# Kernel optimization log

Hardware: AMD Instinct MI355X
Metric: run time of the kernel (lower is better)

The kernel has to match this reference:

```python
import jax, jax.numpy as jnp
import numpy as np

EMBED = 768
HEADS = 12
HEAD_DIM = EMBED // HEADS
HIDDEN = 4 * EMBED


def layer_norm(x, gamma, beta, eps=1e-5):
    mu = jnp.mean(x, axis=-1, keepdims=True)
    var = jnp.var(x, axis=-1, keepdims=True)
    return (x - mu) * jax.lax.rsqrt(var + eps) * gamma + beta


def setup_inputs() -> dict:
    key = jax.random.key(0)
    ks = jax.random.split(key, 10)
    B, N, C = 64, 577, EMBED
    s_in = 1.0 / np.sqrt(C)
    s_hid = 1.0 / np.sqrt(HIDDEN)
    return {
        "x": jax.random.normal(ks[0], (B, N, C), jnp.float32),
        "ln1_g": jnp.ones((C,), jnp.float32),
        "ln1_b": jnp.zeros((C,), jnp.float32),
        "w_qkv": jax.random.normal(ks[1], (C, 3 * C), jnp.float32) * s_in,  # no bias (qkv_bias=False)
        "w_proj": jax.random.normal(ks[2], (C, C), jnp.float32) * s_in,
        "b_proj": jnp.zeros((C,), jnp.float32),
        "ln2_g": jnp.ones((C,), jnp.float32),
        "ln2_b": jnp.zeros((C,), jnp.float32),
        "w_fc1": jax.random.normal(ks[3], (C, HIDDEN), jnp.float32) * s_in,
        "b_fc1": jnp.zeros((HIDDEN,), jnp.float32),
        "w_fc2": jax.random.normal(ks[4], (HIDDEN, C), jnp.float32) * s_hid,
        "b_fc2": jnp.zeros((C,), jnp.float32),
    }


def reference(x, ln1_g, ln1_b, w_qkv, w_proj, b_proj, ln2_g, ln2_b, w_fc1, b_fc1, w_fc2, b_fc2):
    B, N, C = x.shape
    # --- attention branch (pre-norm) ---
    h = layer_norm(x, ln1_g, ln1_b)
    qkv = (h @ w_qkv).reshape(B, N, 3, HEADS, HEAD_DIM)
    q = jnp.transpose(qkv[:, :, 0], (0, 2, 1, 3))  # [B,H,N,D]
    k = jnp.transpose(qkv[:, :, 1], (0, 2, 1, 3))
    v = jnp.transpose(qkv[:, :, 2], (0, 2, 1, 3))
    scale = HEAD_DIM ** -0.5
    att = jax.nn.softmax(jnp.einsum("bhnd,bhmd->bhnm", q, k) * scale, axis=-1)
    o = jnp.einsum("bhnm,bhmd->bhnd", att, v)
    o = jnp.transpose(o, (0, 2, 1, 3)).reshape(B, N, C)
    x = x + (o @ w_proj + b_proj)
    # --- MLP branch (pre-norm) ---
    h = layer_norm(x, ln2_g, ln2_b)
    h = jax.nn.gelu(h @ w_fc1 + b_fc1, approximate=False)
    x = x + (h @ w_fc2 + b_fc2)
    return x
```

## Files before the change

### kernel.cpp

```cpp
#include <hip/hip_runtime.h>
#include <hip/hip_bf16.h>
#include <math.h>

using bf16 = __hip_bfloat16;
typedef __attribute__((ext_vector_type(8))) short short8;
typedef __attribute__((ext_vector_type(4))) float f32x4;

#define NSEQ   577
#define NBATCH 64
#define NTOK   36928
#define MPAD   37120
#define NHEADS 12
#define HDIM   64
#define NP     640
#define CEMB   768
#define CHID   3072
#define NBH    (NBATCH*NHEADS)

__device__ __forceinline__ bf16 f2bf(float v){ return __float2bfloat16(v); }

__device__ __forceinline__ float gelu_f(float x) {
    float x3 = x * x * x;
    float y = 1.5957691216057308f * (x + 0.044715f * x3);
    float e = __expf(y);
    float t = 1.0f - 2.0f / (e + 1.0f);
    return 0.5f * x * (1.0f + t);
}

#define GLOAD_LDS16(gaddr, laddr) \
  __builtin_amdgcn_global_load_lds((__attribute__((address_space(1))) const void*)(gaddr), \
                                   (__attribute__((address_space(3))) void*)(laddr), 16, 0, 0)

__global__ __launch_bounds__(256) void transpose_w(const float* __restrict__ src,
                                                   bf16* __restrict__ dst, int R, int C) {
    long idx = (long)blockIdx.x * 256 + threadIdx.x;
    long total = (long)R * C;
    if (idx < total) {
        int r = (int)(idx / C);
        int c = (int)(idx - (long)r * C);
        dst[(long)c * R + r] = f2bf(src[idx]);
    }
}

__global__ __launch_bounds__(256) void ln_kernel(const float* __restrict__ x,
                                                 const float* __restrict__ gamma,
                                                 const float* __restrict__ beta,
                                                 bf16* __restrict__ out) {
    int row = blockIdx.x;
    const float* xr = x + (size_t)row * CEMB;
    int tid = threadIdx.x;
    float v0 = xr[tid], v1 = xr[tid + 256], v2 = xr[tid + 512];
    float s = v0 + v1 + v2;
    #pragma unroll
    for (int o = 32; o > 0; o >>= 1) s += __shfl_down(s, o);
    __shared__ float red[4];
    if ((tid & 63) == 0) red[tid >> 6] = s;
    __syncthreads();
    float mean = (red[0] + red[1] + red[2] + red[3]) * (1.0f / CEMB);
    float d0 = v0 - mean, d1 = v1 - mean, d2 = v2 - mean;
    float q = d0*d0 + d1*d1 + d2*d2;
    #pragma unroll
    for (int o = 32; o > 0; o >>= 1) q += __shfl_down(q, o);
    __shared__ float red2[4];
    if ((tid & 63) == 0) red2[tid >> 6] = q;
    __syncthreads();
    float var = (red2[0] + red2[1] + red2[2] + red2[3]) * (1.0f / CEMB);
    float rs = rsqrtf(var + 1e-5f);
    bf16* orow = out + (size_t)row * CEMB;
    orow[tid]       = f2bf(d0 * rs * gamma[tid]       + beta[tid]);
    orow[tid + 256] = f2bf(d1 * rs * gamma[tid + 256] + beta[tid + 256]);
    orow[tid + 512] = f2bf(d2 * rs * gamma[tid + 512] + beta[tid + 512]);
}

__global__ __launch_bounds__(256) void flash_attn(const bf16* __restrict__ qg,
                                                  const bf16* __restrict__ kg,
                                                  const bf16* __restrict__ vtg,
                                                  bf16* __restrict__ og) {
    const int tid = threadIdx.x, lane = tid & 63, w = tid >> 6;
    const int fr = lane & 15, fh = lane >> 4;
    const int bh = blockIdx.y;
    const int q0 = blockIdx.x * 128;
    const int wr = w * 32;

    __shared__ bf16 Ks[64 * 64];
    __shared__ bf16 Vs[64 * 64];
    __shared__ bf16 Ps[128 * 64];

    const bf16* qb = qg  + (size_t)bh * NP * HDIM;
    const bf16* kb = kg  + (size_t)bh * NP * HDIM;
    const bf16* vb = vtg + (size_t)bh * HDIM * NP;

    short8 qa[2][2];
    #pragma unroll
    for (int mi = 0; mi < 2; mi++)
        #pragma unroll
        for (int ks = 0; ks < 2; ks++)
            qa[mi][ks] = *reinterpret_cast<const short8*>(
                qb + (size_t)(q0 + wr + mi * 16 + fr) * HDIM + ks * 32 + fh * 8);

    f32x4 od[2][4] = {};
    float m_run[2][4], l_run[2][4];
    #pragma unroll
    for (int mi = 0; mi < 2; mi++)
        #pragma unroll
        for (int r = 0; r < 4; r++) { m_run[mi][r] = -1e30f; l_run[mi][r] = 0.f; }

    for (int t = 0; t < NP / 64; t++) {
        const int kb0 = t * 64;
        __syncthreads();
        {
            const bf16* src = kb + (size_t)kb0 * HDIM;
            GLOAD_LDS16(src + w * 512 + lane * 8,        Ks + w * 512);
            GLOAD_LDS16(src + 2048 + w * 512 + lane * 8, Ks + 2048 + w * 512);
        }
        {
            int d0 = w * 8;
            GLOAD_LDS16(vb + (size_t)(d0 + (lane >> 3)) * NP + kb0 + (lane & 7) * 8,
                        Vs + d0 * 64);
            d0 = 32 + w * 8;
            GLOAD_LDS16(vb + (size_t)(d0 + (lane >> 3)) * NP + kb0 + (lane & 7) * 8,
                        Vs + d0 * 64);
        }
        __syncthreads();

        f32x4 sacc[2][4] = {};
        short8 kf[4][2];
        #pragma unroll
        for (int n = 0; n < 4; n++)
            #pragma unroll
            for (int ks = 0; ks < 2; ks++)
                kf[n][ks] = *reinterpret_cast<const short8*>(&Ks[(n * 16 + fr) * 64 + ks * 32 + fh * 8]);
        #pragma unroll
        for (int mi = 0; mi < 2; mi++)
            #pragma unroll
            for (int n = 0; n < 4; n++)
                #pragma unroll
                for (int ks = 0; ks < 2; ks++)
                    sacc[mi][n] = __builtin_amdgcn_mfma_f32_16x16x32_bf16(qa[mi][ks], kf[n][ks], sacc[mi][n], 0, 0, 0);

        #pragma unroll
        for (int mi = 0; mi < 2; mi++) {
            float sv[4][4];
            float tm[4] = {-1e30f, -1e30f, -1e30f, -1e30f};
            #pragma unroll
            for (int n = 0; n < 4; n++) {
                int col = kb0 + n * 16 + fr;
                bool valid = col < NSEQ;
                #pragma unroll
                for (int r = 0; r < 4; r++) {
                    float s = sacc[mi][n][r];
                    sv[n][r] = valid ? s : -1e30f;
                    tm[r] = fmaxf(tm[r], sv[n][r]);
                }
            }
            #pragma unroll
            for (int r = 0; r < 4; r++) {
                #pragma unroll
                for (int o = 1; o < 16; o <<= 1) tm[r] = fmaxf(tm[r], __shfl_xor(tm[r], o));
                float mn = fmaxf(m_run[mi][r], tm[r]);
                float sc = __expf(m_run[mi][r] - mn);
                m_run[mi][r] = mn;
                float ps = 0.f;
                #pragma unroll
                for (int n = 0; n < 4; n++) {
                    float e = __expf(sv[n][r] - mn);
                    sv[n][r] = e; ps += e;
                }
                #pragma unroll
                for (int o = 1; o < 16; o <<= 1) ps += __shfl_xor(ps, o);
                l_run[mi][r] = l_run[mi][r] * sc + ps;
                #pragma unroll
                for (int n2 = 0; n2 < 4; n2++) od[mi][n2][r] *= sc;
            }
            #pragma unroll
            for (int n = 0; n < 4; n++)
                #pragma unroll
                for (int r = 0; r < 4; r++)
                    Ps[(wr + mi * 16 + fh * 4 + r) * 64 + n * 16 + fr] = f2bf(sv[n][r]);
        }
        __syncthreads();

        short8 pa[2][2], vf[4][2];
        #pragma unroll
        for (int mi = 0; mi < 2; mi++)
            #pragma unroll
            for (int ks = 0; ks < 2; ks++)
                pa[mi][ks] = *reinterpret_cast<const short8*>(&Ps[(wr + mi * 16 + fr) * 64 + ks * 32 + fh * 8]);
        #pragma unroll
        for (int n2 = 0; n2 < 4; n2++)
            #pragma unroll
            for (int ks = 0; ks < 2; ks++)
                vf[n2][ks] = *reinterpret_cast<const short8*>(&Vs[(n2 * 16 + fr) * 64 + ks * 32 + fh * 8]);
        #pragma unroll
        for (int mi = 0; mi < 2; mi++)
            #pragma unroll
            for (int n2 = 0; n2 < 4; n2++)
                #pragma unroll
                for (int ks = 0; ks < 2; ks++)
                    od[mi][n2] = __builtin_amdgcn_mfma_f32_16x16x32_bf16(pa[mi][ks], vf[n2][ks], od[mi][n2], 0, 0, 0);
    }

    const int b = bh / NHEADS, hh = bh - b * NHEADS;
    #pragma unroll
    for (int mi = 0; mi < 2; mi++)
        #pragma unroll
        for (int r = 0; r < 4; r++) {
            int qrow = q0 + wr + mi * 16 + fh * 4 + r;
            if (qrow < NSEQ) {
                float inv = 1.f / l_run[mi][r];
                #pragma unroll
                for (int n2 = 0; n2 < 4; n2++)
                    og[((size_t)(b * NSEQ + qrow)) * CEMB + hh * HDIM + n2 * 16 + fr] =
                        f2bf(od[mi][n2][r] * inv);
            }
        }
}

#define MODE_QKV  1
#define MODE_PROJ 3
#define MODE_FC1  4
#define MODE_FC2  5

struct GemmParams {
    const bf16* A;
    const bf16* Bt;
    int M, N, K;
    int Mreal;
    float* Cf;
    bf16* Cb;
    const float* bias;
    const float* resid;
    bf16* qb; bf16* kb; bf16* vtb;
};

template<int MODE>
__global__ __launch_bounds__(512, 2) void gemm256(GemmParams p) {
    __shared__ bf16 AsBuf[2][256 * 64];
    __shared__ bf16 BsBuf[2][256 * 64];
    const int tid  = threadIdx.x;
    const int lane = tid & 63;
    const int w    = tid >> 6;

    const int gx = gridDim.x, gy = gridDim.y;
    const int nwg = gx * gy;
    const int orig = blockIdx.y * gx + blockIdx.x;
    const int q8 = nwg >> 3, r8 = nwg & 7;
    const int xcd = orig & 7, oid = orig >> 3;
    const int lin2 = ((xcd < r8) ? xcd * (q8 + 1) : r8 * (q8 + 1) + (xcd - r8) * q8) + oid;
    const int bm = (lin2 / gy) * 256;
    const int bn = (lin2 % gy) * 256;

    const int Kd = p.K;
    const int wm = w >> 2, wn = w & 3;
    const int wr = wm * 128, wc = wn * 64;
    const int fr = lane & 15;
    const int fk = (lane >> 4) * 8;

    const int sr = w * 8 + (lane >> 3);
    const int sc = (lane & 7) * 8;
    const bf16* aS[4]; const bf16* bS[4];
    #pragma unroll
    for (int s = 0; s < 4; s++) {
        aS[s] = p.A  + (size_t)(bm + s * 64 + sr) * Kd + sc;
        bS[s] = p.Bt + (size_t)(bn + s * 64 + sr) * Kd + sc;
    }

    f32x4 acc[8][4] = {};
    bf16 *Ac = AsBuf[0], *An = AsBuf[1], *Bc = BsBuf[0], *Bn = BsBuf[1];

    auto stage = [&](bf16* Ad, bf16* Bd) {
        #pragma unroll
        for (int s = 0; s < 4; s++) {
            GLOAD_LDS16(aS[s], Ad + (size_t)(s * 8 + w) * 512);
            GLOAD_LDS16(bS[s], Bd + (size_t)(s * 8 + w) * 512);
            aS[s] += 64; bS[s] += 64;
        }
    };
    auto compute = [&](const bf16* Ad, const bf16* Bd) {
        #pragma unroll
        for (int ks = 0; ks < 2; ks++) {
            short8 b[4];
            #pragma unroll
            for (int n = 0; n < 4; n++)
                b[n] = *reinterpret_cast<const short8*>(&Bd[(wc + n * 16 + fr) * 64 + ks * 32 + fk]);
            #pragma unroll
            for (int m = 0; m < 8; m++) {
                short8 a = *reinterpret_cast<const short8*>(&Ad[(wr + m * 16 + fr) * 64 + ks * 32 + fk]);
                #pragma unroll
                for (int n = 0; n < 4; n++)
                    acc[m][n] = __builtin_amdgcn_mfma_f32_16x16x32_bf16(a, b[n], acc[m][n], 0, 0, 0);
            }
        }
    };

    const int T = Kd >> 6;
    stage(Ac, Bc);
    __syncthreads();
    for (int t = 1; t < T; ++t) {
        stage(An, Bn);
        compute(Ac, Bc);
        __syncthreads();
        bf16* tp;
        tp = Ac; Ac = An; An = tp;
        tp = Bc; Bc = Bn; Bn = tp;
    }
    compute(Ac, Bc);

    const int fq = (lane >> 4) * 4;
    const int colw = bn + wc;

    if (MODE == MODE_QKV) {
        const int which = colw / CEMB;
        const int hh = (colw - which * CEMB) >> 6;
        const float scl = (which == 0) ? 0.125f : 1.0f;
        #pragma unroll
        for (int m = 0; m < 8; m++)
        #pragma unroll
        for (int r = 0; r < 4; r++) {
            int row = bm + wr + m * 16 + fq + r;
            if (row < p.Mreal) {
                int b2 = row / NSEQ;
                int n2 = row - b2 * NSEQ;
                size_t bh = (size_t)b2 * NHEADS + hh;
                if (which == 0) {
                    bf16* dst = p.qb + (bh * NP + n2) * HDIM + fr;
                    #pragma unroll
                    for (int n = 0; n < 4; n++) dst[n * 16] = f2bf(acc[m][n][r] * scl);
                } else if (which == 1) {
                    bf16* dst = p.kb + (bh * NP + n2) * HDIM + fr;
                    #pragma unroll
                    for (int n = 0; n < 4; n++) dst[n * 16] = f2bf(acc[m][n][r]);
                } else {
                    bf16* dst = p.vtb + (bh * HDIM + fr) * NP + n2;
                    #pragma unroll
                    for (int n = 0; n < 4; n++) dst[(size_t)n * 16 * NP] = f2bf(acc[m][n][r]);
                }
            }
        }
    } else if (MODE == MODE_FC1) {
        const float* bp = p.bias + colw + fr;
        float bb[4];
        #pragma unroll
        for (int n = 0; n < 4; n++) bb[n] = bp[n * 16];
        #pragma unroll
        for (int m = 0; m < 8; m++)
        #pragma unroll
        for (int r = 0; r < 4; r++) {
            int row = bm + wr + m * 16 + fq + r;
            if (row < p.Mreal) {
                bf16* crow = p.Cb + (size_t)row * p.N + colw + fr;
                #pragma unroll
                for (int n = 0; n < 4; n++)
                    crow[n * 16] = f2bf(gelu_f(acc[m][n][r] + bb[n]));
            }
        }
    } else {
        const float* bp = p.bias + colw + fr;
        float bb[4];
        #pragma unroll
        for (int n = 0; n < 4; n++) bb[n] = bp[n * 16];
        #pragma unroll
        for (int m = 0; m < 8; m++)
        #pragma unroll
        for (int r = 0; r < 4; r++) {
            int row = bm + wr + m * 16 + fq + r;
            if (row < p.Mreal) {
                float* crow = p.Cf + (size_t)row * p.N + colw + fr;
                const float* rrow = p.resid + (size_t)row * p.N + colw + fr;
                #pragma unroll
                for (int n = 0; n < 4; n++)
                    crow[n * 16] = acc[m][n][r] + bb[n] + rrow[n * 16];
            }
        }
    }
}

extern "C" void kernel_launch(void* const* d_in, const int* in_sizes, int n_in,
                              void* d_out, int out_size, void* d_ws, size_t ws_size,
                              hipStream_t stream) {
    const float* x      = (const float*)d_in[0];
    const float* ln1_g  = (const float*)d_in[1];
    const float* ln1_b  = (const float*)d_in[2];
    const float* w_qkv  = (const float*)d_in[3];
    const float* w_proj = (const float*)d_in[4];
    const float* b_proj = (const float*)d_in[5];
    const float* ln2_g  = (const float*)d_in[6];
    const float* ln2_b  = (const float*)d_in[7];
    const float* w_fc1  = (const float*)d_in[8];
    const float* b_fc1  = (const float*)d_in[9];
    const float* w_fc2  = (const float*)d_in[10];
    const float* b_fc2  = (const float*)d_in[11];
    float* out = (float*)d_out;

    char* ws = (char*)d_ws;
    auto al = [](size_t b){ return (b + 255) & ~(size_t)255; };
    size_t off = 0;
    auto take = [&](size_t b)->char* { char* p = ws + off; off += al(b); return p; };

    bf16* wqkvT  = (bf16*)take((size_t)2304 * 768 * 2);
    bf16* wprojT = (bf16*)take((size_t)768 * 768 * 2);
    bf16* wfc1T  = (bf16*)take((size_t)3072 * 768 * 2);
    bf16* wfc2T  = (bf16*)take((size_t)768 * 3072 * 2);
    bf16* h      = (bf16*)take((size_t)MPAD * CEMB * 2);
    bf16* o      = (bf16*)take((size_t)MPAD * CEMB * 2);
    size_t fixedEnd = off;

    const size_t qkvB = (size_t)NBH * NP * HDIM * 2;
    bf16* q_c  = (bf16*)(ws + fixedEnd);
    bf16* k_c  = (bf16*)(ws + fixedEnd + qkvB);
    bf16* vT_c = (bf16*)(ws + fixedEnd + 2 * qkvB);
    bf16* g_c  = (bf16*)(ws + fixedEnd);

    transpose_w<<<(768 * 2304 + 255) / 256, 256, 0, stream>>>(w_qkv, wqkvT, 768, 2304);
    transpose_w<<<(768 * 768 + 255) / 256, 256, 0, stream>>>(w_proj, wprojT, 768, 768);
    transpose_w<<<(768 * 3072 + 255) / 256, 256, 0, stream>>>(w_fc1, wfc1T, 768, 3072);
    transpose_w<<<(3072 * 768 + 255) / 256, 256, 0, stream>>>(w_fc2, wfc2T, 3072, 768);

    ln_kernel<<<NTOK, 256, 0, stream>>>(x, ln1_g, ln1_b, h);

    {
        GemmParams p{};
        p.A = h; p.Bt = wqkvT;
        p.M = MPAD; p.N = 3 * CEMB; p.K = CEMB; p.Mreal = NTOK;
        p.qb = q_c; p.kb = k_c; p.vtb = vT_c;
        gemm256<MODE_QKV><<<dim3(MPAD / 256, 3 * CEMB / 256), 512, 0, stream>>>(p);
    }

    flash_attn<<<dim3(NP / 128, NBH), 256, 0, stream>>>(q_c, k_c, vT_c, o);

    {
        GemmParams p{};
        p.A = o; p.Bt = wprojT;
        p.M = MPAD; p.N = CEMB; p.K = CEMB; p.Mreal = NTOK;
        p.Cf = out; p.bias = b_proj; p.resid = x;
        gemm256<MODE_PROJ><<<dim3(MPAD / 256, CEMB / 256), 512, 0, stream>>>(p);
    }

    ln_kernel<<<NTOK, 256, 0, stream>>>(out, ln2_g, ln2_b, h);

    {
        GemmParams p{};
        p.A = h; p.Bt = wfc1T;
        p.M = MPAD; p.N = CHID; p.K = CEMB; p.Mreal = NTOK;
        p.Cb = g_c; p.bias = b_fc1;
        gemm256<MODE_FC1><<<dim3(MPAD / 256, CHID / 256), 512, 0, stream>>>(p);
    }

    {
        GemmParams p{};
        p.A = g_c; p.Bt = wfc2T;
        p.M = MPAD; p.N = CEMB; p.K = CHID; p.Mreal = NTOK;
        p.Cf = out; p.bias = b_fc2; p.resid = out;
        gemm256<MODE_FC2><<<dim3(MPAD / 256, CEMB / 256), 512, 0, stream>>>(p);
    }
}
```

Measured before the change: 1.377 ms.

## Swizzle flash-attention LDS tiles, add lazy softmax rescale and MFMA priority

Applies an XOR swizzle to the K, V and P tiles in shared memory, both on the global-to-LDS loads and on the fragment reads, to cut LDS bank conflicts. Softmax rescaling of the running max, sum and output accumulator now happens only when the new tile max exceeds the old one by more than 8, which skips the exp and multiplies in most iterations. s_setprio is raised around the MFMA blocks to favour matrix issue across waves. The lazy rescale lets exponentials reach up to e^8 before rescaling, which lowers the precision margin of the bf16 P values.

```diff
diff --git a/kernel.cpp b/kernel.cpp
--- a/kernel.cpp
+++ b/kernel.cpp
@@ -90,6 +90,10 @@
     const bf16* kb = kg  + (size_t)bh * NP * HDIM;
     const bf16* vb = vtg + (size_t)bh * HDIM * NP;
 
+    const int swz  = (fr & 7) << 3;
+    const int scol = (((lane & 7) ^ (lane >> 3)) << 3);
+    const int srow = lane >> 3;
+
     short8 qa[2][2];
     #pragma unroll
     for (int mi = 0; mi < 2; mi++)
@@ -108,19 +112,10 @@
     for (int t = 0; t < NP / 64; t++) {
         const int kb0 = t * 64;
         __syncthreads();
-        {
-            const bf16* src = kb + (size_t)kb0 * HDIM;
-            GLOAD_LDS16(src + w * 512 + lane * 8,        Ks + w * 512);
-            GLOAD_LDS16(src + 2048 + w * 512 + lane * 8, Ks + 2048 + w * 512);
-        }
-        {
-            int d0 = w * 8;
-            GLOAD_LDS16(vb + (size_t)(d0 + (lane >> 3)) * NP + kb0 + (lane & 7) * 8,
-                        Vs + d0 * 64);
-            d0 = 32 + w * 8;
-            GLOAD_LDS16(vb + (size_t)(d0 + (lane >> 3)) * NP + kb0 + (lane & 7) * 8,
-                        Vs + d0 * 64);
-        }
+        GLOAD_LDS16(kb + (size_t)(kb0 + w * 8 + srow) * HDIM + scol,      Ks + w * 512);
+        GLOAD_LDS16(kb + (size_t)(kb0 + 32 + w * 8 + srow) * HDIM + scol, Ks + 2048 + w * 512);
+        GLOAD_LDS16(vb + (size_t)(w * 8 + srow) * NP + kb0 + scol,        Vs + w * 512);
+        GLOAD_LDS16(vb + (size_t)(32 + w * 8 + srow) * NP + kb0 + scol,   Vs + 2048 + w * 512);
         __syncthreads();
 
         f32x4 sacc[2][4] = {};
@@ -129,7 +124,9 @@
         for (int n = 0; n < 4; n++)
             #pragma unroll
             for (int ks = 0; ks < 2; ks++)
-                kf[n][ks] = *reinterpret_cast<const short8*>(&Ks[(n * 16 + fr) * 64 + ks * 32 + fh * 8]);
+                kf[n][ks] = *reinterpret_cast<const short8*>(
+                    &Ks[(n * 16 + fr) * 64 + ((ks * 32 + fh * 8) ^ swz)]);
+        __builtin_amdgcn_s_setprio(1);
         #pragma unroll
         for (int mi = 0; mi < 2; mi++)
             #pragma unroll
@@ -137,6 +134,7 @@
                 #pragma unroll
                 for (int ks = 0; ks < 2; ks++)
                     sacc[mi][n] = __builtin_amdgcn_mfma_f32_16x16x32_bf16(qa[mi][ks], kf[n][ks], sacc[mi][n], 0, 0, 0);
+        __builtin_amdgcn_s_setprio(0);
 
         #pragma unroll
         for (int mi = 0; mi < 2; mi++) {
@@ -157,26 +155,31 @@
             for (int r = 0; r < 4; r++) {
                 #pragma unroll
                 for (int o = 1; o < 16; o <<= 1) tm[r] = fmaxf(tm[r], __shfl_xor(tm[r], o));
-                float mn = fmaxf(m_run[mi][r], tm[r]);
-                float sc = __expf(m_run[mi][r] - mn);
-                m_run[mi][r] = mn;
+                float mo = m_run[mi][r];
+                if (tm[r] - mo > 8.f) {
+                    float sc = __expf(mo - tm[r]);
+                    mo = tm[r];
+                    m_run[mi][r] = mo;
+                    l_run[mi][r] *= sc;
+                    #pragma unroll
+                    for (int n2 = 0; n2 < 4; n2++) od[mi][n2][r] *= sc;
+                }
                 float ps = 0.f;
                 #pragma unroll
                 for (int n = 0; n < 4; n++) {
-                    float e = __expf(sv[n][r] - mn);
+                    float e = __expf(sv[n][r] - mo);
                     sv[n][r] = e; ps += e;
                 }
                 #pragma unroll
                 for (int o = 1; o < 16; o <<= 1) ps += __shfl_xor(ps, o);
-                l_run[mi][r] = l_run[mi][r] * sc + ps;
-                #pragma unroll
-                for (int n2 = 0; n2 < 4; n2++) od[mi][n2][r] *= sc;
+                l_run[mi][r] += ps;
             }
             #pragma unroll
             for (int n = 0; n < 4; n++)
                 #pragma unroll
                 for (int r = 0; r < 4; r++)
-                    Ps[(wr + mi * 16 + fh * 4 + r) * 64 + n * 16 + fr] = f2bf(sv[n][r]);
+                    Ps[(wr + mi * 16 + fh * 4 + r) * 64 +
+                       ((n * 16 + fr) ^ (((fh * 4 + r) & 7) << 3))] = f2bf(sv[n][r]);
         }
         __syncthreads();
 
@@ -185,12 +188,15 @@
         for (int mi = 0; mi < 2; mi++)
             #pragma unroll
             for (int ks = 0; ks < 2; ks++)
-                pa[mi][ks] = *reinterpret_cast<const short8*>(&Ps[(wr + mi * 16 + fr) * 64 + ks * 32 + fh * 8]);
+                pa[mi][ks] = *reinterpret_cast<const short8*>(
+                    &Ps[(wr + mi * 16 + fr) * 64 + ((ks * 32 + fh * 8) ^ swz)]);
         #pragma unroll
         for (int n2 = 0; n2 < 4; n2++)
             #pragma unroll
             for (int ks = 0; ks < 2; ks++)
-                vf[n2][ks] = *reinterpret_cast<const short8*>(&Vs[(n2 * 16 + fr) * 64 + ks * 32 + fh * 8]);
+                vf[n2][ks] = *reinterpret_cast<const short8*>(
+                    &Vs[(n2 * 16 + fr) * 64 + ((ks * 32 + fh * 8) ^ swz)]);
+        __builtin_amdgcn_s_setprio(1);
         #pragma unroll
         for (int mi = 0; mi < 2; mi++)
             #pragma unroll
@@ -198,6 +204,7 @@
                 #pragma unroll
                 for (int ks = 0; ks < 2; ks++)
                     od[mi][n2] = __builtin_amdgcn_mfma_f32_16x16x32_bf16(pa[mi][ks], vf[n2][ks], od[mi][n2], 0, 0, 0);
+        __builtin_amdgcn_s_setprio(0);
     }
 
     const int b = bh / NHEADS, hh = bh - b * NHEADS;
```

After: 1.381 ms. No clear change (+0.3%).
